# Optimization experiments

Measured on AMD Instinct MI355X. Metric: run time of the kernel, lower is better.

The kernel has to match this reference:

```python
import jax, jax.numpy as jnp
import numpy as np

NUM_USERS = 100000
NUM_ITEMS = 200000
EMBED_DIM = 64
NUM_LAYERS = 3
NNZ = 4000000
BATCH = 16384
N_TOTAL = NUM_USERS + NUM_ITEMS


def setup_inputs() -> dict:
    key = jax.random.key(0)
    k = jax.random.split(key, 7)
    user_ids = jax.random.randint(k[0], (BATCH,), 0, NUM_USERS, dtype=jnp.int32)
    item_ids = jax.random.randint(k[1], (BATCH,), 0, NUM_ITEMS, dtype=jnp.int32)
    adj_row = jax.random.randint(k[2], (NNZ,), 0, N_TOTAL, dtype=jnp.int32)
    adj_col = jax.random.randint(k[3], (NNZ,), 0, N_TOTAL, dtype=jnp.int32)
    # normalized-adjacency-like positive values (D^-1/2 A D^-1/2 entries)
    adj_val = jax.random.uniform(k[4], (NNZ,), dtype=jnp.float32) * 0.1
    user_emb_w = jax.random.normal(k[5], (NUM_USERS, EMBED_DIM), dtype=jnp.float32) * 0.1
    item_emb_w = jax.random.normal(k[6], (NUM_ITEMS, EMBED_DIM), dtype=jnp.float32) * 0.1
    return {"user_ids": user_ids, "item_ids": item_ids, "adj_row": adj_row,
            "adj_col": adj_col, "adj_val": adj_val,
            "user_emb_w": user_emb_w, "item_emb_w": item_emb_w}


def _spmm(row, col, val, x):
    # y = A @ x for COO sparse A: gather source rows, scale, scatter-add to dest rows
    msgs = x[col] * val[:, None]  # [nnz, D]
    return jax.ops.segment_sum(msgs, row, num_segments=N_TOTAL)


def reference(user_ids, item_ids, adj_row, adj_col, adj_val, user_emb_w, item_emb_w):
    all_emb = jnp.concatenate([user_emb_w, item_emb_w], axis=0)  # [N+M, D]
    acc = all_emb  # running sum over K+1 layer embeddings (== stack+mean)
    x = all_emb
    for _ in range(NUM_LAYERS):
        x = _spmm(adj_row, adj_col, adj_val, x)
        acc = acc + x
    final = acc / jnp.float32(NUM_LAYERS + 1)
    u = final[user_ids]                    # [B, D]
    i = final[item_ids + NUM_USERS]        # [B, D]
    return jnp.sum(u * i, axis=-1)         # [B]
```

## Files before the change

### kernel.cpp

```cpp
#include <hip/hip_runtime.h>

#define NUM_USERS 100000
#define NUM_ITEMS 200000
#define NT        300000
#define D         64
#define NNZ_C     4000000
#define BATCH     16384

#define SB_LOG    10
#define SB_ROWS   1024
#define NSB       ((NT + SB_ROWS - 1) / SB_ROWS)
#define SBCAP     16384
#define CHUNK     8192
#define NCHUNK    ((NNZ_C + CHUNK - 1) / CHUNK)

__global__ void p1_bin(const int* __restrict__ row, const int* __restrict__ col,
                       const float* __restrict__ val, int* __restrict__ bcnt,
                       int2* __restrict__ entries) {
    __shared__ int hist[NSB];
    __shared__ int cur[NSB];
    int tid = threadIdx.x;
    long cb = (long)blockIdx.x * CHUNK;
    int n = (int)((NNZ_C - cb < CHUNK) ? (NNZ_C - cb) : CHUNK);
    for (int i = tid; i < NSB; i += 512) hist[i] = 0;
    __syncthreads();
    for (int k = tid; k < n; k += 512)
        atomicAdd(&hist[row[cb + k] >> SB_LOG], 1);
    __syncthreads();
    for (int i = tid; i < NSB; i += 512)
        cur[i] = atomicAdd(&bcnt[i], hist[i]);
    __syncthreads();
    for (int k = tid; k < n; k += 512) {
        int r = row[cb + k];
        int b = r >> SB_LOG;
        int pos = atomicAdd(&cur[b], 1);
        if (pos < SBCAP)
            entries[(long)b * SBCAP + pos] =
                make_int2(col[cb + k] | ((r & (SB_ROWS - 1)) << 19),
                          __float_as_int(val[cb + k]));
    }
}

__global__ void bucket_scan(const int* __restrict__ bcnt, int* __restrict__ bucketstart,
                            int* __restrict__ rowstart) {
    __shared__ int s[512];
    int tid = threadIdx.x;
    int v = (tid < NSB) ? min(bcnt[tid], SBCAP) : 0;
    int acc = v;
    s[tid] = acc; __syncthreads();
    for (int off = 1; off < 512; off <<= 1) {
        int t = (tid >= off) ? s[tid - off] : 0;
        __syncthreads();
        acc += t; s[tid] = acc; __syncthreads();
    }
    if (tid < NSB) bucketstart[tid] = acc - v;
    if (tid == 0) rowstart[NT] = s[511];
}

__global__ void p2_csr(const int* __restrict__ bcnt, const int* __restrict__ bucketstart,
                       const int2* __restrict__ entries, int* __restrict__ rowstart,
                       int2* __restrict__ cv) {
    __shared__ int h[SB_ROWS];
    __shared__ int cur[SB_ROWS];
    int b = blockIdx.x, tid = threadIdx.x;
    int n = min(bcnt[b], SBCAP);
    const int2* eb = entries + (long)b * SBCAP;
    h[tid] = 0; __syncthreads();
    for (int k = tid; k < n; k += SB_ROWS)
        atomicAdd(&h[((unsigned)eb[k].x) >> 19], 1);
    __syncthreads();
    int v = h[tid];
    int acc = v;
    __syncthreads();
    for (int off = 1; off < SB_ROWS; off <<= 1) {
        int t = (tid >= off) ? h[tid - off] : 0;
        __syncthreads();
        acc += t; h[tid] = acc; __syncthreads();
    }
    int rs = bucketstart[b] + (acc - v);
    int grow = (b << SB_LOG) + tid;
    if (grow < NT) rowstart[grow] = rs;
    cur[tid] = rs;
    __syncthreads();
    for (int k = tid; k < n; k += SB_ROWS) {
        int2 e = eb[k];
        int rl = ((unsigned)e.x) >> 19;
        int p = atomicAdd(&cur[rl], 1);
        cv[p] = make_int2(e.x & 0x7FFFF, e.y);
    }
}

__global__ void mark_needed(const int* __restrict__ uid, const int* __restrict__ iid,
                            const int* __restrict__ rowstart, const int2* __restrict__ cv,
                            char* __restrict__ flags) {
    int t = blockIdx.x * blockDim.x + threadIdx.x;
    int r = (t < BATCH) ? uid[t] : (iid[t - BATCH] + NUM_USERS);
    flags[r] = 1;
    int e = rowstart[r + 1];
    for (int j = rowstart[r]; j < e; ++j)
        flags[cv[j].x] = 1;
}

template <bool CAT>
__device__ inline const float* xaddr(const float* __restrict__ x,
                                     const float* __restrict__ uw,
                                     const float* __restrict__ iw, int c) {
    if (CAT)
        return (c < NUM_USERS) ? (uw + (long)c * D) : (iw + (long)(c - NUM_USERS) * D);
    return x + (long)c * D;
}

template <bool CAT, bool FILT>
__global__ void csr_spmm_k(const int* __restrict__ rowstart, const int2* __restrict__ cv,
                           const float* __restrict__ x, const float* __restrict__ uw,
                           const float* __restrict__ iw, const char* __restrict__ flags,
                           float* __restrict__ y) {
    int r = blockIdx.x * 4 + (threadIdx.x >> 6);
    if (r >= NT) return;
    if (FILT && !flags[r]) return;
    int lane = threadIdx.x & 63;
    int grp = lane >> 4, sub = lane & 15;
    int s = rowstart[r], e = rowstart[r + 1];
    float4 a = make_float4(0.f, 0.f, 0.f, 0.f);
    float4 b = make_float4(0.f, 0.f, 0.f, 0.f);
    for (int j = s; j < e; j += 8) {
        int i0 = j + grp, i1 = j + 4 + grp;
        int2 p0 = cv[(i0 < e) ? i0 : (e - 1)];
        int2 p1 = cv[(i1 < e) ? i1 : (e - 1)];
        float v0 = (i0 < e) ? __int_as_float(p0.y) : 0.f;
        float v1 = (i1 < e) ? __int_as_float(p1.y) : 0.f;
        const float* xp0 = xaddr<CAT>(x, uw, iw, p0.x);
        const float* xp1 = xaddr<CAT>(x, uw, iw, p1.x);
        float4 g0 = *(const float4*)(xp0 + sub * 4);
        float4 g1 = *(const float4*)(xp1 + sub * 4);
        a.x += v0 * g0.x; a.y += v0 * g0.y; a.z += v0 * g0.z; a.w += v0 * g0.w;
        b.x += v1 * g1.x; b.y += v1 * g1.y; b.z += v1 * g1.z; b.w += v1 * g1.w;
    }
    a.x += b.x; a.y += b.y; a.z += b.z; a.w += b.w;
    a.x += __shfl_xor(a.x, 16); a.y += __shfl_xor(a.y, 16);
    a.z += __shfl_xor(a.z, 16); a.w += __shfl_xor(a.w, 16);
    a.x += __shfl_xor(a.x, 32); a.y += __shfl_xor(a.y, 32);
    a.z += __shfl_xor(a.z, 32); a.w += __shfl_xor(a.w, 32);
    if (grp == 0) ((float4*)(y + (long)r * D))[sub] = a;
}

__global__ void csr_spmm_acc(const int* __restrict__ uid, const int* __restrict__ iid,
                             const int* __restrict__ rowstart, const int2* __restrict__ cv,
                             const float* __restrict__ x, float* __restrict__ acc) {
    int bidx = blockIdx.x * 4 + (threadIdx.x >> 6);
    if (bidx >= 2 * BATCH) return;
    int lane = threadIdx.x & 63;
    int grp = lane >> 4, sub = lane & 15;
    int r = (bidx < BATCH) ? uid[bidx] : (iid[bidx - BATCH] + NUM_USERS);
    int s = rowstart[r], e = rowstart[r + 1];
    float4 a = make_float4(0.f, 0.f, 0.f, 0.f);
    float4 b = make_float4(0.f, 0.f, 0.f, 0.f);
    for (int j = s; j < e; j += 8) {
        int i0 = j + grp, i1 = j + 4 + grp;
        int2 p0 = cv[(i0 < e) ? i0 : (e - 1)];
        int2 p1 = cv[(i1 < e) ? i1 : (e - 1)];
        float v0 = (i0 < e) ? __int_as_float(p0.y) : 0.f;
        float v1 = (i1 < e) ? __int_as_float(p1.y) : 0.f;
        float4 g0 = *(const float4*)(x + (long)p0.x * D + sub * 4);
        float4 g1 = *(const float4*)(x + (long)p1.x * D + sub * 4);
        a.x += v0 * g0.x; a.y += v0 * g0.y; a.z += v0 * g0.z; a.w += v0 * g0.w;
        b.x += v1 * g1.x; b.y += v1 * g1.y; b.z += v1 * g1.z; b.w += v1 * g1.w;
    }
    a.x += b.x; a.y += b.y; a.z += b.z; a.w += b.w;
    a.x += __shfl_xor(a.x, 16); a.y += __shfl_xor(a.y, 16);
    a.z += __shfl_xor(a.z, 16); a.w += __shfl_xor(a.w, 16);
    a.x += __shfl_xor(a.x, 32); a.y += __shfl_xor(a.y, 32);
    a.z += __shfl_xor(a.z, 32); a.w += __shfl_xor(a.w, 32);
    if (grp == 0) {
        float4* ap = (float4*)(acc + (long)bidx * D) + sub;
        float4 p = *ap;
        p.x += a.x; p.y += a.y; p.z += a.z; p.w += a.w;
        *ap = p;
    }
}

__global__ void gather_init(const int* __restrict__ uid, const int* __restrict__ iid,
                            const float* __restrict__ uw, const float* __restrict__ iw,
                            float* __restrict__ acc) {
    int t = blockIdx.x * blockDim.x + threadIdx.x;
    int b   = t >> 4;
    int sub = t & 15;
    const float* src = (b < BATCH) ? (uw + (long)uid[b] * D)
                                   : (iw + (long)iid[b - BATCH] * D);
    ((float4*)(acc + (long)b * D))[sub] = ((const float4*)src)[sub];
}

__global__ void gather_acc(const int* __restrict__ uid, const int* __restrict__ iid,
                           const float* __restrict__ x, float* __restrict__ acc) {
    int t = blockIdx.x * blockDim.x + threadIdx.x;
    int b   = t >> 4;
    int sub = t & 15;
    int r   = (b < BATCH) ? uid[b] : (iid[b - BATCH] + NUM_USERS);
    float4 g = *((const float4*)(x + (long)r * D) + sub);
    float4* a = (float4*)(acc + (long)b * D) + sub;
    float4 p = *a;
    p.x += g.x; p.y += g.y; p.z += g.z; p.w += g.w;
    *a = p;
}

__global__ void final_dot(const float* __restrict__ acc, float* __restrict__ out) {
    int t = blockIdx.x * blockDim.x + threadIdx.x;
    int b   = t >> 4;
    int sub = t & 15;
    float4 u = *((const float4*)(acc + (long)b * D) + sub);
    float4 w = *((const float4*)(acc + (long)(b + BATCH) * D) + sub);
    float p = u.x * w.x + u.y * w.y + u.z * w.z + u.w * w.w;
    p += __shfl_xor(p, 1);
    p += __shfl_xor(p, 2);
    p += __shfl_xor(p, 4);
    p += __shfl_xor(p, 8);
    if (sub == 0) out[b] = p * (1.0f / 16.0f);
}

extern "C" void kernel_launch(void* const* d_in, const int* in_sizes, int n_in,
                              void* d_out, int out_size, void* d_ws, size_t ws_size,
                              hipStream_t stream) {
    const int*   user_ids = (const int*)d_in[0];
    const int*   item_ids = (const int*)d_in[1];
    const int*   adj_row  = (const int*)d_in[2];
    const int*   adj_col  = (const int*)d_in[3];
    const float* adj_val  = (const float*)d_in[4];
    const float* uw       = (const float*)d_in[5];
    const float* iw       = (const float*)d_in[6];
    float*       out      = (float*)d_out;

    char* ws = (char*)d_ws;
    size_t off = 0;
    auto alloc = [&](size_t bytes) {
        char* p = ws + off;
        off += (bytes + 255) & ~(size_t)255;
        return p;
    };
    const size_t xbytes = (size_t)NT * D * sizeof(float);
    float* xA          = (float*)alloc(xbytes);
    float* xB          = (float*)alloc(xbytes);
    float* acc         = (float*)alloc((size_t)2 * BATCH * D * sizeof(float));
    int*   rowstart    = (int*)alloc((size_t)(NT + 1) * sizeof(int));
    int*   bcnt        = (int*)alloc((size_t)NSB * sizeof(int));
    int*   bucketstart = (int*)alloc((size_t)NSB * sizeof(int));
    char*  flags       = (char*)alloc((size_t)NT);
    int2*  cv          = (int2*)alloc((size_t)NNZ_C * sizeof(int2));
    int2*  entries     = (int2*)xB;

    hipMemsetAsync(bcnt, 0, (size_t)NSB * sizeof(int), stream);
    p1_bin<<<NCHUNK, 512, 0, stream>>>(adj_row, adj_col, adj_val, bcnt, entries);
    bucket_scan<<<1, 512, 0, stream>>>(bcnt, bucketstart, rowstart);
    p2_csr<<<NSB, SB_ROWS, 0, stream>>>(bcnt, bucketstart, entries, rowstart, cv);

    hipMemsetAsync(flags, 0, (size_t)NT, stream);
    mark_needed<<<(2 * BATCH) / 256, 256, 0, stream>>>(user_ids, item_ids, rowstart, cv, flags);

    gather_init<<<(2 * BATCH * 16) / 256, 256, 0, stream>>>(user_ids, item_ids, uw, iw, acc);

    csr_spmm_k<true, false><<<(NT + 3) / 4, 256, 0, stream>>>(rowstart, cv, nullptr, uw, iw,
                                                              nullptr, xA);
    gather_acc<<<(2 * BATCH * 16) / 256, 256, 0, stream>>>(user_ids, item_ids, xA, acc);

    csr_spmm_k<false, true><<<(NT + 3) / 4, 256, 0, stream>>>(rowstart, cv, xA, nullptr, nullptr,
                                                              flags, xB);
    gather_acc<<<(2 * BATCH * 16) / 256, 256, 0, stream>>>(user_ids, item_ids, xB, acc);

    csr_spmm_acc<<<(2 * BATCH + 3) / 4, 256, 0, stream>>>(user_ids, item_ids,
                                                          rowstart, cv, xB, acc);

    final_dot<<<(BATCH * 16) / 256, 256, 0, stream>>>(acc, out);
}
```

Before: 586.3 us.

## Store intermediate layer embeddings in fp16 to halve SpMM gather traffic

```diff
diff --git a/kernel.cpp b/kernel.cpp
--- a/kernel.cpp
+++ b/kernel.cpp
@@ -1,4 +1,5 @@
 #include <hip/hip_runtime.h>
+#include <hip/hip_fp16.h>
 
 #define NUM_USERS 100000
 #define NUM_ITEMS 200000
@@ -13,6 +14,19 @@
 #define SBCAP     16384
 #define CHUNK     8192
 #define NCHUNK    ((NNZ_C + CHUNK - 1) / CHUNK)
+
+__device__ inline void fma8(float4& a, float4& b, float v, uint4 g) {
+    const __half2* h = (const __half2*)&g;
+    float2 f0 = __half22float2(h[0]); a.x += v * f0.x; a.y += v * f0.y;
+    float2 f1 = __half22float2(h[1]); a.z += v * f1.x; a.w += v * f1.y;
+    float2 f2 = __half22float2(h[2]); b.x += v * f2.x; b.y += v * f2.y;
+    float2 f3 = __half22float2(h[3]); b.z += v * f3.x; b.w += v * f3.y;
+}
+
+__device__ inline unsigned pack2(float x, float y) {
+    __half2 h = __floats2half2_rn(x, y);
+    return *(unsigned*)&h;
+}
 
 __global__ void p1_bin(const int* __restrict__ row, const int* __restrict__ col,
                        const float* __restrict__ val, int* __restrict__ bcnt,
@@ -101,81 +115,99 @@
         flags[cv[j].x] = 1;
 }
 
-template <bool CAT>
-__device__ inline const float* xaddr(const float* __restrict__ x,
-                                     const float* __restrict__ uw,
-                                     const float* __restrict__ iw, int c) {
-    if (CAT)
-        return (c < NUM_USERS) ? (uw + (long)c * D) : (iw + (long)(c - NUM_USERS) * D);
-    return x + (long)c * D;
-}
-
-template <bool CAT, bool FILT>
-__global__ void csr_spmm_k(const int* __restrict__ rowstart, const int2* __restrict__ cv,
-                           const float* __restrict__ x, const float* __restrict__ uw,
-                           const float* __restrict__ iw, const char* __restrict__ flags,
-                           float* __restrict__ y) {
+__global__ void init_x0(const float* __restrict__ uw, const float* __restrict__ iw,
+                        unsigned short* __restrict__ x0) {
+    int t = blockIdx.x * blockDim.x + threadIdx.x;
+    int r = t >> 3, sub = t & 7;
+    const float* src = (r < NUM_USERS) ? (uw + (long)r * D)
+                                       : (iw + (long)(r - NUM_USERS) * D);
+    float4 f0 = ((const float4*)src)[sub * 2];
+    float4 f1 = ((const float4*)src)[sub * 2 + 1];
+    uint4 o;
+    o.x = pack2(f0.x, f0.y); o.y = pack2(f0.z, f0.w);
+    o.z = pack2(f1.x, f1.y); o.w = pack2(f1.z, f1.w);
+    ((uint4*)(x0 + (long)r * D))[sub] = o;
+}
+
+template <bool FILT>
+__global__ void csr_spmm_h(const int* __restrict__ rowstart, const int2* __restrict__ cv,
+                           const unsigned short* __restrict__ x,
+                           const char* __restrict__ flags,
+                           unsigned short* __restrict__ y) {
     int r = blockIdx.x * 4 + (threadIdx.x >> 6);
     if (r >= NT) return;
     if (FILT && !flags[r]) return;
     int lane = threadIdx.x & 63;
-    int grp = lane >> 4, sub = lane & 15;
+    int grp = lane >> 3, sub = lane & 7;
     int s = rowstart[r], e = rowstart[r + 1];
-    float4 a = make_float4(0.f, 0.f, 0.f, 0.f);
-    float4 b = make_float4(0.f, 0.f, 0.f, 0.f);
-    for (int j = s; j < e; j += 8) {
-        int i0 = j + grp, i1 = j + 4 + grp;
+    float4 a0 = make_float4(0.f, 0.f, 0.f, 0.f), a1 = a0;
+    float4 b0 = a0, b1 = a0;
+    for (int j = s; j < e; j += 16) {
+        int i0 = j + grp, i1 = j + 8 + grp;
         int2 p0 = cv[(i0 < e) ? i0 : (e - 1)];
         int2 p1 = cv[(i1 < e) ? i1 : (e - 1)];
         float v0 = (i0 < e) ? __int_as_float(p0.y) : 0.f;
         float v1 = (i1 < e) ? __int_as_float(p1.y) : 0.f;
-        const float* xp0 = xaddr<CAT>(x, uw, iw, p0.x);
-        const float* xp1 = xaddr<CAT>(x, uw, iw, p1.x);
-        float4 g0 = *(const float4*)(xp0 + sub * 4);
-        float4 g1 = *(const float4*)(xp1 + sub * 4);
-        a.x += v0 * g0.x; a.y += v0 * g0.y; a.z += v0 * g0.z; a.w += v0 * g0.w;
-        b.x += v1 * g1.x; b.y += v1 * g1.y; b.z += v1 * g1.z; b.w += v1 * g1.w;
-    }
-    a.x += b.x; a.y += b.y; a.z += b.z; a.w += b.w;
-    a.x += __shfl_xor(a.x, 16); a.y += __shfl_xor(a.y, 16);
-    a.z += __shfl_xor(a.z, 16); a.w += __shfl_xor(a.w, 16);
-    a.x += __shfl_xor(a.x, 32); a.y += __shfl_xor(a.y, 32);
-    a.z += __shfl_xor(a.z, 32); a.w += __shfl_xor(a.w, 32);
-    if (grp == 0) ((float4*)(y + (long)r * D))[sub] = a;
-}
-
-__global__ void csr_spmm_acc(const int* __restrict__ uid, const int* __restrict__ iid,
-                             const int* __restrict__ rowstart, const int2* __restrict__ cv,
-                             const float* __restrict__ x, float* __restrict__ acc) {
+        uint4 g0 = *(const uint4*)(x + (long)p0.x * D + sub * 8);
+        uint4 g1 = *(const uint4*)(x + (long)p1.x * D + sub * 8);
+        fma8(a0, a1, v0, g0);
+        fma8(b0, b1, v1, g1);
+    }
+    a0.x += b0.x; a0.y += b0.y; a0.z += b0.z; a0.w += b0.w;
+    a1.x += b1.x; a1.y += b1.y; a1.z += b1.z; a1.w += b1.w;
+    #pragma unroll
+    for (int off = 8; off <= 32; off <<= 1) {
+        a0.x += __shfl_xor(a0.x, off); a0.y += __shfl_xor(a0.y, off);
+        a0.z += __shfl_xor(a0.z, off); a0.w += __shfl_xor(a0.w, off);
+        a1.x += __shfl_xor(a1.x, off); a1.y += __shfl_xor(a1.y, off);
+        a1.z += __shfl_xor(a1.z, off); a1.w += __shfl_xor(a1.w, off);
+    }
+    if (grp == 0) {
+        uint4 o;
+        o.x = pack2(a0.x, a0.y); o.y = pack2(a0.z, a0.w);
+        o.z = pack2(a1.x, a1.y); o.w = pack2(a1.z, a1.w);
+        ((uint4*)(y + (long)r * D))[sub] = o;
+    }
+}
+
+__global__ void csr_spmm_acc_h(const int* __restrict__ uid, const int* __restrict__ iid,
+                               const int* __restrict__ rowstart, const int2* __restrict__ cv,
+                               const unsigned short* __restrict__ x,
+                               float* __restrict__ acc) {
     int bidx = blockIdx.x * 4 + (threadIdx.x >> 6);
     if (bidx >= 2 * BATCH) return;
     int lane = threadIdx.x & 63;
-    int grp = lane >> 4, sub = lane & 15;
+    int grp = lane >> 3, sub = lane & 7;
     int r = (bidx < BATCH) ? uid[bidx] : (iid[bidx - BATCH] + NUM_USERS);
     int s = rowstart[r], e = rowstart[r + 1];
-    float4 a = make_float4(0.f, 0.f, 0.f, 0.f);
-    float4 b = make_float4(0.f, 0.f, 0.f, 0.f);
-    for (int j = s; j < e; j += 8) {
-        int i0 = j + grp, i1 = j + 4 + grp;
+    float4 a0 = make_float4(0.f, 0.f, 0.f, 0.f), a1 = a0;
+    float4 b0 = a0, b1 = a0;
+    for (int j = s; j < e; j += 16) {
+        int i0 = j + grp, i1 = j + 8 + grp;
         int2 p0 = cv[(i0 < e) ? i0 : (e - 1)];
         int2 p1 = cv[(i1 < e) ? i1 : (e - 1)];
         float v0 = (i0 < e) ? __int_as_float(p0.y) : 0.f;
         float v1 = (i1 < e) ? __int_as_float(p1.y) : 0.f;
-        float4 g0 = *(const float4*)(x + (long)p0.x * D + sub * 4);
-        float4 g1 = *(const float4*)(x + (long)p1.x * D + sub * 4);
-        a.x += v0 * g0.x; a.y += v0 * g0.y; a.z += v0 * g0.z; a.w += v0 * g0.w;
-        b.x += v1 * g1.x; b.y += v1 * g1.y; b.z += v1 * g1.z; b.w += v1 * g1.w;
-    }
-    a.x += b.x; a.y += b.y; a.z += b.z; a.w += b.w;
-    a.x += __shfl_xor(a.x, 16); a.y += __shfl_xor(a.y, 16);
-    a.z += __shfl_xor(a.z, 16); a.w += __shfl_xor(a.w, 16);
-    a.x += __shfl_xor(a.x, 32); a.y += __shfl_xor(a.y, 32);
-    a.z += __shfl_xor(a.z, 32); a.w += __shfl_xor(a.w, 32);
+        uint4 g0 = *(const uint4*)(x + (long)p0.x * D + sub * 8);
+        uint4 g1 = *(const uint4*)(x + (long)p1.x * D + sub * 8);
+        fma8(a0, a1, v0, g0);
+        fma8(b0, b1, v1, g1);
+    }
+    a0.x += b0.x; a0.y += b0.y; a0.z += b0.z; a0.w += b0.w;
+    a1.x += b1.x; a1.y += b1.y; a1.z += b1.z; a1.w += b1.w;
+    #pragma unroll
+    for (int off = 8; off <= 32; off <<= 1) {
+        a0.x += __shfl_xor(a0.x, off); a0.y += __shfl_xor(a0.y, off);
+        a0.z += __shfl_xor(a0.z, off); a0.w += __shfl_xor(a0.w, off);
+        a1.x += __shfl_xor(a1.x, off); a1.y += __shfl_xor(a1.y, off);
+        a1.z += __shfl_xor(a1.z, off); a1.w += __shfl_xor(a1.w, off);
+    }
     if (grp == 0) {
-        float4* ap = (float4*)(acc + (long)bidx * D) + sub;
-        float4 p = *ap;
-        p.x += a.x; p.y += a.y; p.z += a.z; p.w += a.w;
-        *ap = p;
+        float4* ap = (float4*)(acc + (long)bidx * D) + sub * 2;
+        float4 q0 = ap[0], q1 = ap[1];
+        q0.x += a0.x; q0.y += a0.y; q0.z += a0.z; q0.w += a0.w;
+        q1.x += a1.x; q1.y += a1.y; q1.z += a1.z; q1.w += a1.w;
+        ap[0] = q0; ap[1] = q1;
     }
 }
 
@@ -190,17 +222,21 @@
     ((float4*)(acc + (long)b * D))[sub] = ((const float4*)src)[sub];
 }
 
-__global__ void gather_acc(const int* __restrict__ uid, const int* __restrict__ iid,
-                           const float* __restrict__ x, float* __restrict__ acc) {
-    int t = blockIdx.x * blockDim.x + threadIdx.x;
-    int b   = t >> 4;
-    int sub = t & 15;
+__global__ void gather_acc_h(const int* __restrict__ uid, const int* __restrict__ iid,
+                             const unsigned short* __restrict__ x, float* __restrict__ acc) {
+    int t = blockIdx.x * blockDim.x + threadIdx.x;
+    int b   = t >> 3;
+    int sub = t & 7;
     int r   = (b < BATCH) ? uid[b] : (iid[b - BATCH] + NUM_USERS);
-    float4 g = *((const float4*)(x + (long)r * D) + sub);
-    float4* a = (float4*)(acc + (long)b * D) + sub;
-    float4 p = *a;
-    p.x += g.x; p.y += g.y; p.z += g.z; p.w += g.w;
-    *a = p;
+    uint4 g = ((const uint4*)(x + (long)r * D))[sub];
+    const __half2* h = (const __half2*)&g;
+    float4* ap = (float4*)(acc + (long)b * D) + sub * 2;
+    float4 q0 = ap[0], q1 = ap[1];
+    float2 f0 = __half22float2(h[0]); q0.x += f0.x; q0.y += f0.y;
+    float2 f1 = __half22float2(h[1]); q0.z += f1.x; q0.w += f1.y;
+    float2 f2 = __half22float2(h[2]); q1.x += f2.x; q1.y += f2.y;
+    float2 f3 = __half22float2(h[3]); q1.z += f3.x; q1.w += f3.y;
+    ap[0] = q0; ap[1] = q1;
 }
 
 __global__ void final_dot(const float* __restrict__ acc, float* __restrict__ out) {
@@ -236,16 +272,18 @@
         off += (bytes + 255) & ~(size_t)255;
         return p;
     };
-    const size_t xbytes = (size_t)NT * D * sizeof(float);
-    float* xA          = (float*)alloc(xbytes);
-    float* xB          = (float*)alloc(xbytes);
-    float* acc         = (float*)alloc((size_t)2 * BATCH * D * sizeof(float));
-    int*   rowstart    = (int*)alloc((size_t)(NT + 1) * sizeof(int));
-    int*   bcnt        = (int*)alloc((size_t)NSB * sizeof(int));
-    int*   bucketstart = (int*)alloc((size_t)NSB * sizeof(int));
-    char*  flags       = (char*)alloc((size_t)NT);
-    int2*  cv          = (int2*)alloc((size_t)NNZ_C * sizeof(int2));
-    int2*  entries     = (int2*)xB;
+    const size_t xhbytes = (size_t)NT * D * sizeof(unsigned short);
+    const size_t ebytes  = (size_t)NSB * SBCAP * sizeof(int2);
+    unsigned short* x0h = (unsigned short*)alloc(xhbytes);
+    unsigned short* xAh = (unsigned short*)alloc(xhbytes);
+    unsigned short* xBh = (unsigned short*)alloc(ebytes > xhbytes ? ebytes : xhbytes);
+    float* acc          = (float*)alloc((size_t)2 * BATCH * D * sizeof(float));
+    int*   rowstart     = (int*)alloc((size_t)(NT + 1) * sizeof(int));
+    int*   bcnt         = (int*)alloc((size_t)NSB * sizeof(int));
+    int*   bucketstart  = (int*)alloc((size_t)NSB * sizeof(int));
+    char*  flags        = (char*)alloc((size_t)NT);
+    int2*  cv           = (int2*)alloc((size_t)NNZ_C * sizeof(int2));
+    int2*  entries      = (int2*)xBh;
 
     hipMemsetAsync(bcnt, 0, (size_t)NSB * sizeof(int), stream);
     p1_bin<<<NCHUNK, 512, 0, stream>>>(adj_row, adj_col, adj_val, bcnt, entries);
@@ -255,18 +293,17 @@
     hipMemsetAsync(flags, 0, (size_t)NT, stream);
     mark_needed<<<(2 * BATCH) / 256, 256, 0, stream>>>(user_ids, item_ids, rowstart, cv, flags);
 
+    init_x0<<<(NT * 8) / 256, 256, 0, stream>>>(uw, iw, x0h);
     gather_init<<<(2 * BATCH * 16) / 256, 256, 0, stream>>>(user_ids, item_ids, uw, iw, acc);
 
-    csr_spmm_k<true, false><<<(NT + 3) / 4, 256, 0, stream>>>(rowstart, cv, nullptr, uw, iw,
-                                                              nullptr, xA);
-    gather_acc<<<(2 * BATCH * 16) / 256, 256, 0, stream>>>(user_ids, item_ids, xA, acc);
-
-    csr_spmm_k<false, true><<<(NT + 3) / 4, 256, 0, stream>>>(rowstart, cv, xA, nullptr, nullptr,
-                                                              flags, xB);
-    gather_acc<<<(2 * BATCH * 16) / 256, 256, 0, stream>>>(user_ids, item_ids, xB, acc);
-
-    csr_spmm_acc<<<(2 * BATCH + 3) / 4, 256, 0, stream>>>(user_ids, item_ids,
-                                                          rowstart, cv, xB, acc);
+    csr_spmm_h<false><<<(NT + 3) / 4, 256, 0, stream>>>(rowstart, cv, x0h, nullptr, xAh);
+    gather_acc_h<<<(2 * BATCH * 8) / 256, 256, 0, stream>>>(user_ids, item_ids, xAh, acc);
+
+    csr_spmm_h<true><<<(NT + 3) / 4, 256, 0, stream>>>(rowstart, cv, xAh, flags, xBh);
+    gather_acc_h<<<(2 * BATCH * 8) / 256, 256, 0, stream>>>(user_ids, item_ids, xBh, acc);
+
+    csr_spmm_acc_h<<<(2 * BATCH + 3) / 4, 256, 0, stream>>>(user_ids, item_ids,
+                                                            rowstart, cv, xBh, acc);
 
     final_dot<<<(BATCH * 16) / 256, 256, 0, stream>>>(acc, out);
 }
```

New measurement: 511.6 us. 1.15x faster.
